# Kernel optimization log

Measured on AMD Instinct MI355X. Metric: run time of the kernel, lower is better.

The kernel has to match this reference:

```python
import jax, jax.numpy as jnp
import numpy as np

NEG_INF = -1e30  # stand-in for float('-inf'); avoids NaNs if a row is fully masked


def setup_inputs() -> dict:
    key = jax.random.key(0)
    k1, k2, k3, k4 = jax.random.split(key, 4)
    B, Q, K, D = 16, 2048, 2048, 64
    query = jax.random.normal(k1, (B, Q, D), dtype=jnp.float32)
    key_t = jax.random.normal(k2, (B, K, D), dtype=jnp.float32)
    value = jax.random.normal(k3, (B, K, D), dtype=jnp.float32)
    mask = jax.random.randint(k4, (B, Q, K), 0, 2).astype(jnp.bool_)
    return {"query": query, "key": key_t, "value": value, "mask": mask}


def reference(query, key, value, mask):
    d = query.shape[-1]
    # [B,Q,K] score matrix (naive attention, as in the original module)
    score = jnp.einsum('bqd,bkd->bqk', query, key) / jnp.sqrt(jnp.asarray(d, query.dtype))
    score = jnp.where(mask, NEG_INF, score)  # masked_fill(mask, -inf)
    attn = jax.nn.softmax(score, axis=-1)
    # dropout p=0.0 -> identity
    return jnp.einsum('bqk,bkd->bqd', attn, value)
```

## Files before the change

kernel.cpp:

```cpp
#include <hip/hip_runtime.h>


#define Bn   16
#define Qn   2048
#define Kseq 2048
#define Dn   64
#define QBLK 128
#define NEGF (-1e30f)

typedef __attribute__((ext_vector_type(8)))  short short8;
typedef __attribute__((ext_vector_type(16))) float f32x16;

static __device__ __forceinline__ short f2bf(float x) {
  union { float f; unsigned u; } un; un.f = x;
  unsigned r = un.u + 0x7FFFu + ((un.u >> 16) & 1u);
  return (short)(r >> 16);
}
static __device__ __forceinline__ unsigned pkbf(float lo, float hi) {
  unsigned r;
  asm("v_cvt_pk_bf16_f32 %0, %1, %2" : "=v"(r) : "v"(lo), "v"(hi));
  return r;
}
#if __has_builtin(__builtin_amdgcn_exp2f)
#define EXP2 __builtin_amdgcn_exp2f
#else
#define EXP2 exp2f
#endif
#define MFMA32 __builtin_amdgcn_mfma_f32_32x32x16_bf16

#define PREFETCH(MNXT)                                                        \
  do {                                                                        \
    ka0 = *(const float4*)(kp);                                               \
    ka1 = *(const float4*)(kp + 4);                                           \
    kb0 = *(const float4*)(kp + 2048);                                        \
    kb1 = *(const float4*)(kp + 2052);                                        \
    _Pragma("unroll")                                                         \
    for (int j = 0; j < 16; ++j) vreg[j] = vp[j * 64];                        \
    _Pragma("unroll")                                                         \
    for (int g = 0; g < 8; ++g) MNXT[g] = mp[2 * g];                          \
    kp += 4096; vp += 4096; mp += 16;                                         \
  } while (0)

#define WRITELDS()                                                            \
  do {                                                                        \
    short8 t;                                                                 \
    t[0]=f2bf(ka0.x); t[1]=f2bf(ka0.y); t[2]=f2bf(ka0.z); t[3]=f2bf(ka0.w);   \
    t[4]=f2bf(ka1.x); t[5]=f2bf(ka1.y); t[6]=f2bf(ka1.z); t[7]=f2bf(ka1.w);   \
    *(short8*)kwa = t;                                                        \
    t[0]=f2bf(kb0.x); t[1]=f2bf(kb0.y); t[2]=f2bf(kb0.z); t[3]=f2bf(kb0.w);   \
    t[4]=f2bf(kb1.x); t[5]=f2bf(kb1.y); t[6]=f2bf(kb1.z); t[7]=f2bf(kb1.w);   \
    *(short8*)kwb = t;                                                        \
    short8 v0, v1;                                                            \
    _Pragma("unroll")                                                         \
    for (int j = 0; j < 8; ++j) { v0[j]=f2bf(vreg[j]); v1[j]=f2bf(vreg[8+j]); } \
    *(short8*)vwa = v0; *(short8*)vwb = v1;                                   \
  } while (0)

#define COMPUTE(MCUR)                                                         \
  do {                                                                        \
    f32x16 st0, st1;                                                          \
    _Pragma("unroll")                                                         \
    for (int i = 0; i < 16; ++i) { st0[i] = 0.f; st1[i] = 0.f; }              \
    _Pragma("unroll")                                                         \
    for (int s = 0; s < 4; ++s) {                                             \
      short8 kf = *(const short8*)(krd + ((32*s + hh) ^ swz));                \
      st0 = MFMA32(kf, qf[s], st0, 0, 0, 0);                                  \
      short8 kg = *(const short8*)(krd + 4096 + ((32*s + hh) ^ swz));         \
      st1 = MFMA32(kg, qf[s], st1, 0, 0, 0);                                  \
    }                                                                         \
    float p0[16], p1[16];                                                     \
    _Pragma("unroll")                                                         \
    for (int g = 0; g < 4; ++g) {                                             \
      int4 m0 = MCUR[g]; int4 m1 = MCUR[4 + g];                               \
      p0[4*g+0] = m0.x ? NEGF : st0[4*g+0];                                   \
      p0[4*g+1] = m0.y ? NEGF : st0[4*g+1];                                   \
      p0[4*g+2] = m0.z ? NEGF : st0[4*g+2];                                   \
      p0[4*g+3] = m0.w ? NEGF : st0[4*g+3];                                   \
      p1[4*g+0] = m1.x ? NEGF : st1[4*g+0];                                   \
      p1[4*g+1] = m1.y ? NEGF : st1[4*g+1];                                   \
      p1[4*g+2] = m1.z ? NEGF : st1[4*g+2];                                   \
      p1[4*g+3] = m1.w ? NEGF : st1[4*g+3];                                   \
    }                                                                         \
    float mx8[8];                                                             \
    _Pragma("unroll")                                                         \
    for (int i = 0; i < 8; ++i)                                               \
      mx8[i] = fmaxf(fmaxf(p0[i], p0[i+8]), fmaxf(p1[i], p1[i+8]));           \
    float mx = fmaxf(fmaxf(fmaxf(mx8[0],mx8[1]), fmaxf(mx8[2],mx8[3])),       \
                     fmaxf(fmaxf(mx8[4],mx8[5]), fmaxf(mx8[6],mx8[7])));      \
    mx = fmaxf(mx, __shfl_xor(mx, 32));                                       \
    if (!__all(mx <= mrun)) {                                                 \
      float mnew  = fmaxf(mrun, mx);                                          \
      float alpha = EXP2(mrun - mnew);                                        \
      lrun *= alpha;                                                          \
      _Pragma("unroll")                                                       \
      for (int i = 0; i < 16; ++i) { ot0[i] *= alpha; ot1[i] *= alpha; }      \
      mrun = mnew;                                                            \
    }                                                                         \
    _Pragma("unroll")                                                         \
    for (int i = 0; i < 16; ++i) {                                            \
      p0[i] = EXP2(p0[i] - mrun);                                             \
      p1[i] = EXP2(p1[i] - mrun);                                             \
    }                                                                         \
    float s8[8];                                                              \
    _Pragma("unroll")                                                         \
    for (int i = 0; i < 8; ++i) s8[i] = (p0[i]+p0[i+8]) + (p1[i]+p1[i+8]);    \
    float lsum = ((s8[0]+s8[1]) + (s8[2]+s8[3])) +                            \
                 ((s8[4]+s8[5]) + (s8[6]+s8[7]));                             \
    lsum += __shfl_xor(lsum, 32);                                             \
    lrun += lsum;                                                             \
    union U8 { unsigned u[4]; short8 s; } f0, f1, f2, f3;                     \
    {                                                                         \
      unsigned x0 = pkbf(p0[0],p0[1]),   x1 = pkbf(p0[2],p0[3]);              \
      unsigned y0 = pkbf(p0[4],p0[5]),   y1 = pkbf(p0[6],p0[7]);              \
      unsigned a0 = pkbf(p0[8],p0[9]),   a1 = pkbf(p0[10],p0[11]);            \
      unsigned b0 = pkbf(p0[12],p0[13]), b1 = pkbf(p0[14],p0[15]);            \
      unsigned sx0 = __shfl_xor(x0,32), sx1 = __shfl_xor(x1,32);              \
      unsigned sy0 = __shfl_xor(y0,32), sy1 = __shfl_xor(y1,32);              \
      unsigned sa0 = __shfl_xor(a0,32), sa1 = __shfl_xor(a1,32);              \
      unsigned sb0 = __shfl_xor(b0,32), sb1 = __shfl_xor(b1,32);              \
      f0.u[0] = h ? sy0 : x0;  f0.u[1] = h ? sy1 : x1;                        \
      f0.u[2] = h ? y0 : sx0;  f0.u[3] = h ? y1 : sx1;                        \
      f1.u[0] = h ? sb0 : a0;  f1.u[1] = h ? sb1 : a1;                        \
      f1.u[2] = h ? b0 : sa0;  f1.u[3] = h ? b1 : sa1;                        \
    }                                                                         \
    {                                                                         \
      unsigned x0 = pkbf(p1[0],p1[1]),   x1 = pkbf(p1[2],p1[3]);              \
      unsigned y0 = pkbf(p1[4],p1[5]),   y1 = pkbf(p1[6],p1[7]);              \
      unsigned a0 = pkbf(p1[8],p1[9]),   a1 = pkbf(p1[10],p1[11]);            \
      unsigned b0 = pkbf(p1[12],p1[13]), b1 = pkbf(p1[14],p1[15]);            \
      unsigned sx0 = __shfl_xor(x0,32), sx1 = __shfl_xor(x1,32);              \
      unsigned sy0 = __shfl_xor(y0,32), sy1 = __shfl_xor(y1,32);              \
      unsigned sa0 = __shfl_xor(a0,32), sa1 = __shfl_xor(a1,32);              \
      unsigned sb0 = __shfl_xor(b0,32), sb1 = __shfl_xor(b1,32);              \
      f2.u[0] = h ? sy0 : x0;  f2.u[1] = h ? sy1 : x1;                        \
      f2.u[2] = h ? y0 : sx0;  f2.u[3] = h ? y1 : sx1;                        \
      f3.u[0] = h ? sb0 : a0;  f3.u[1] = h ? sb1 : a1;                        \
      f3.u[2] = h ? b0 : sa0;  f3.u[3] = h ? b1 : sa1;                        \
    }                                                                         \
    _Pragma("unroll")                                                         \
    for (int s = 0; s < 4; ++s) {                                             \
      short8 pf = (s==0) ? f0.s : (s==1) ? f1.s : (s==2) ? f2.s : f3.s;       \
      short8 va = *(const short8*)(vrd + ((32*s + hh) ^ swz));                \
      ot0 = MFMA32(va, pf, ot0, 0, 0, 0);                                     \
      short8 vb = *(const short8*)(vrd + 4096 + ((32*s + hh) ^ swz));         \
      ot1 = MFMA32(vb, pf, ot1, 0, 0, 0);                                     \
    }                                                                         \
  } while (0)

__launch_bounds__(256, 1)
__global__ void attn_fused(const float* __restrict__ Qg,
                           const float* __restrict__ Kg,
                           const float* __restrict__ Vg,
                           const int*   __restrict__ Mg,
                           float* __restrict__ Og) {
  __shared__ short8 lds8[1024];
  char* ldsb = (char*)lds8;

  const int tid  = threadIdx.x;
  const int lane = tid & 63;
  const int w    = tid >> 6;
  const int l31  = lane & 31;
  const int h    = lane >> 5;
  const int hh   = h << 4;
  const int swz  = (l31 & 7) << 4;
  const int b    = blockIdx.y;
  const int qb   = blockIdx.x * QBLK;
  const int q    = qb + w * 32 + l31;

  const float qscale = 0.18033688011112042f;
  const float* qp = Qg + ((size_t)(b * Qn + q)) * Dn + 8 * h;
  short8 qf[4];
#pragma unroll
  for (int s = 0; s < 4; ++s) {
    float4 a = *(const float4*)(qp + 16 * s);
    float4 c = *(const float4*)(qp + 16 * s + 4);
    short8 f;
    f[0]=f2bf(a.x*qscale); f[1]=f2bf(a.y*qscale); f[2]=f2bf(a.z*qscale); f[3]=f2bf(a.w*qscale);
    f[4]=f2bf(c.x*qscale); f[5]=f2bf(c.y*qscale); f[6]=f2bf(c.z*qscale); f[7]=f2bf(c.w*qscale);
    qf[s] = f;
  }

  const int krow = tid >> 3, kc8 = tid & 7;
  const float* kp = Kg + ((size_t)b * Kseq + krow) * Dn + kc8 * 8;
  const int vd = tid >> 2, vkc = (tid & 3) << 4;
  const float* vp = Vg + ((size_t)b * Kseq + vkc) * Dn + vd;
  char* kwa = ldsb + krow * 128 + ((kc8 * 16) ^ ((krow & 7) << 4));
  char* kwb = kwa + 32 * 128;
  char* vwa = ldsb + 8192 + vd * 128 + (((vkc * 2)     ) ^ ((vd & 7) << 4));
  char* vwb = ldsb + 8192 + vd * 128 + (((vkc * 2) + 16) ^ ((vd & 7) << 4));
  const char* krd = ldsb + l31 * 128;
  const char* vrd = ldsb + 8192 + l31 * 128;

  const int4* mp = (const int4*)(Mg + ((size_t)(b * Qn + q)) * Kseq) + h;

  f32x16 ot0, ot1;
#pragma unroll
  for (int i = 0; i < 16; ++i) { ot0[i] = 0.f; ot1[i] = 0.f; }
  float mrun = NEGF, lrun = 0.f;

  float4 ka0, ka1, kb0, kb1;
  float  vreg[16];
  int4   ma[8], mb[8];

  PREFETCH(ma);
  WRITELDS();
  __syncthreads();

#pragma unroll 1
  for (int kt = 0; kt < 32; kt += 2) {
    PREFETCH(mb);
    COMPUTE(ma);
    __syncthreads();
    WRITELDS();
    __syncthreads();
    if (kt + 1 < 31) { PREFETCH(ma); }
    COMPUTE(mb);
    __syncthreads();
    if (kt + 1 < 31) { WRITELDS(); }
    __syncthreads();
  }

  float inv = 1.0f / lrun;
  float* op = Og + ((size_t)(b * Qn + q)) * Dn;
#pragma unroll
  for (int g = 0; g < 4; ++g) {
    float4 o;
    o.x = ot0[4*g+0] * inv; o.y = ot0[4*g+1] * inv;
    o.z = ot0[4*g+2] * inv; o.w = ot0[4*g+3] * inv;
    *(float4*)(op + 8*g + 4*h) = o;
    o.x = ot1[4*g+0] * inv; o.y = ot1[4*g+1] * inv;
    o.z = ot1[4*g+2] * inv; o.w = ot1[4*g+3] * inv;
    *(float4*)(op + 32 + 8*g + 4*h) = o;
  }
}

extern "C" void kernel_launch(void* const* d_in, const int* in_sizes, int n_in,
                              void* d_out, int out_size, void* d_ws, size_t ws_size,
                              hipStream_t stream) {
  const float* Q = (const float*)d_in[0];
  const float* K = (const float*)d_in[1];
  const float* V = (const float*)d_in[2];
  const int*   M = (const int*)d_in[3];
  float* O = (float*)d_out;
  dim3 grid(Qn / QBLK, Bn);
  attn_fused<<<grid, dim3(256), 0, stream>>>(Q, K, V, M, O);
}
```

Baseline: 413.2 us.

## Split key range across two wave groups per block with LDS merge of softmax states

Blocks grow from 256 to 512 threads. Two groups of four waves each process alternating 64-key tiles for the same 128 queries, and their online-softmax states (max, sum, output) are merged through LDS at the end. The mask is loaded once per step and compressed into a 32-bit bitmask, replacing the double-buffered int4 mask registers. K/V staging is reorganized so that the single-buffered 32KB LDS holds two K and two V tiles per iteration, which halves the loop count. This raises waves in flight to hide the memory latency of the large mask stream, at the cost of an extra merge phase, more syncs, and register pressure under launch bounds of 512 threads with 2 blocks.

```diff
diff --git a/kernel.cpp b/kernel.cpp
--- a/kernel.cpp
+++ b/kernel.cpp
@@ -8,7 +8,9 @@
 #define QBLK 128
 #define NEGF (-1e30f)
 
+typedef __attribute__((ext_vector_type(4)))  short short4v;
 typedef __attribute__((ext_vector_type(8)))  short short8;
+typedef __attribute__((ext_vector_type(4)))  unsigned uint4v;
 typedef __attribute__((ext_vector_type(16))) float f32x16;
 
 static __device__ __forceinline__ short f2bf(float x) {
@@ -28,63 +30,70 @@
 #endif
 #define MFMA32 __builtin_amdgcn_mfma_f32_32x32x16_bf16
 
-#define PREFETCH(MNXT)                                                        \
-  do {                                                                        \
-    ka0 = *(const float4*)(kp);                                               \
-    ka1 = *(const float4*)(kp + 4);                                           \
-    kb0 = *(const float4*)(kp + 2048);                                        \
-    kb1 = *(const float4*)(kp + 2052);                                        \
-    _Pragma("unroll")                                                         \
-    for (int j = 0; j < 16; ++j) vreg[j] = vp[j * 64];                        \
-    _Pragma("unroll")                                                         \
-    for (int g = 0; g < 8; ++g) MNXT[g] = mp[2 * g];                          \
-    kp += 4096; vp += 4096; mp += 16;                                         \
+#define PREF_KV()                                                             \
+  do {                                                                        \
+    kst[0] = kp4[co0]; kst[1] = kp4[co1];                                     \
+    kst[2] = kp4[co2]; kst[3] = kp4[co3];                                     \
+    _Pragma("unroll")                                                         \
+    for (int j2 = 0; j2 < 8; ++j2) vst[j2] = *(const float2*)(vp + j2 * 64);  \
+    kp4 += 2048; vp += 8192;                                                  \
+  } while (0)
+
+#define PREF_M()                                                              \
+  do {                                                                        \
+    _Pragma("unroll")                                                         \
+    for (int g = 0; g < 8; ++g) ma[g] = mp[2 * g];                            \
+    mp += 32;                                                                 \
   } while (0)
 
 #define WRITELDS()                                                            \
   do {                                                                        \
-    short8 t;                                                                 \
-    t[0]=f2bf(ka0.x); t[1]=f2bf(ka0.y); t[2]=f2bf(ka0.z); t[3]=f2bf(ka0.w);   \
-    t[4]=f2bf(ka1.x); t[5]=f2bf(ka1.y); t[6]=f2bf(ka1.z); t[7]=f2bf(ka1.w);   \
-    *(short8*)kwa = t;                                                        \
-    t[0]=f2bf(kb0.x); t[1]=f2bf(kb0.y); t[2]=f2bf(kb0.z); t[3]=f2bf(kb0.w);   \
-    t[4]=f2bf(kb1.x); t[5]=f2bf(kb1.y); t[6]=f2bf(kb1.z); t[7]=f2bf(kb1.w);   \
-    *(short8*)kwb = t;                                                        \
+    _Pragma("unroll")                                                         \
+    for (int i = 0; i < 4; ++i) {                                             \
+      float4 a = kst[i]; short4v t;                                           \
+      t[0] = f2bf(a.x); t[1] = f2bf(a.y); t[2] = f2bf(a.z); t[3] = f2bf(a.w); \
+      *(short4v*)kdst[i] = t;                                                 \
+    }                                                                         \
     short8 v0, v1;                                                            \
     _Pragma("unroll")                                                         \
-    for (int j = 0; j < 8; ++j) { v0[j]=f2bf(vreg[j]); v1[j]=f2bf(vreg[8+j]); } \
-    *(short8*)vwa = v0; *(short8*)vwb = v1;                                   \
-  } while (0)
-
-#define COMPUTE(MCUR)                                                         \
+    for (int j2 = 0; j2 < 8; ++j2) { v0[j2] = f2bf(vst[j2].x); v1[j2] = f2bf(vst[j2].y); } \
+    *(short8*)vdst0 = v0; *(short8*)vdst1 = v1;                               \
+  } while (0)
+
+static __device__ __forceinline__ unsigned compress_mask(const int4* ma) {
+  unsigned bits = 0;
+#pragma unroll
+  for (int g = 0; g < 8; ++g) {
+    int4 m = ma[g];
+    const int sh = ((g & 4) << 2) + ((g & 3) << 2);
+    unsigned bsel = (m.x != 0 ? 1u : 0u) | (m.y != 0 ? 2u : 0u) |
+                    (m.z != 0 ? 4u : 0u) | (m.w != 0 ? 8u : 0u);
+    bits |= bsel << sh;
+  }
+  return bits;
+}
+
+#define COMPUTE()                                                             \
   do {                                                                        \
     f32x16 st0, st1;                                                          \
     _Pragma("unroll")                                                         \
     for (int i = 0; i < 16; ++i) { st0[i] = 0.f; st1[i] = 0.f; }              \
     _Pragma("unroll")                                                         \
     for (int s = 0; s < 4; ++s) {                                             \
-      short8 kf = *(const short8*)(krd + ((32*s + hh) ^ swz));                \
+      short8 kf = *(const short8*)(krd + ((32 * s + hh) ^ swz));              \
       st0 = MFMA32(kf, qf[s], st0, 0, 0, 0);                                  \
-      short8 kg = *(const short8*)(krd + 4096 + ((32*s + hh) ^ swz));         \
+      short8 kg = *(const short8*)(krd + 4096 + ((32 * s + hh) ^ swz));       \
       st1 = MFMA32(kg, qf[s], st1, 0, 0, 0);                                  \
     }                                                                         \
-    float p0[16], p1[16];                                                     \
-    _Pragma("unroll")                                                         \
-    for (int g = 0; g < 4; ++g) {                                             \
-      int4 m0 = MCUR[g]; int4 m1 = MCUR[4 + g];                               \
-      p0[4*g+0] = m0.x ? NEGF : st0[4*g+0];                                   \
-      p0[4*g+1] = m0.y ? NEGF : st0[4*g+1];                                   \
-      p0[4*g+2] = m0.z ? NEGF : st0[4*g+2];                                   \
-      p0[4*g+3] = m0.w ? NEGF : st0[4*g+3];                                   \
-      p1[4*g+0] = m1.x ? NEGF : st1[4*g+0];                                   \
-      p1[4*g+1] = m1.y ? NEGF : st1[4*g+1];                                   \
-      p1[4*g+2] = m1.z ? NEGF : st1[4*g+2];                                   \
-      p1[4*g+3] = m1.w ? NEGF : st1[4*g+3];                                   \
+    _Pragma("unroll")                                                         \
+    for (int i = 0; i < 16; ++i) {                                            \
+      st0[i] = (bits & (1u << i))       ? NEGF : st0[i];                      \
+      st1[i] = (bits & (0x10000u << i)) ? NEGF : st1[i];                      \
     }                                                                         \
     float mx8[8];                                                             \
     _Pragma("unroll")                                                         \
     for (int i = 0; i < 8; ++i)                                               \
-      mx8[i] = fmaxf(fmaxf(p0[i], p0[i+8]), fmaxf(p1[i], p1[i+8]));           \
+      mx8[i] = fmaxf(fmaxf(st0[i], st0[i+8]), fmaxf(st1[i], st1[i+8]));       \
     float mx = fmaxf(fmaxf(fmaxf(mx8[0],mx8[1]), fmaxf(mx8[2],mx8[3])),       \
                      fmaxf(fmaxf(mx8[4],mx8[5]), fmaxf(mx8[6],mx8[7])));      \
     mx = fmaxf(mx, __shfl_xor(mx, 32));                                       \
@@ -98,74 +107,75 @@
     }                                                                         \
     _Pragma("unroll")                                                         \
     for (int i = 0; i < 16; ++i) {                                            \
-      p0[i] = EXP2(p0[i] - mrun);                                             \
-      p1[i] = EXP2(p1[i] - mrun);                                             \
+      st0[i] = EXP2(st0[i] - mrun);                                           \
+      st1[i] = EXP2(st1[i] - mrun);                                           \
     }                                                                         \
     float s8[8];                                                              \
     _Pragma("unroll")                                                         \
-    for (int i = 0; i < 8; ++i) s8[i] = (p0[i]+p0[i+8]) + (p1[i]+p1[i+8]);    \
+    for (int i = 0; i < 8; ++i) s8[i] = (st0[i]+st0[i+8]) + (st1[i]+st1[i+8]);\
     float lsum = ((s8[0]+s8[1]) + (s8[2]+s8[3])) +                            \
                  ((s8[4]+s8[5]) + (s8[6]+s8[7]));                             \
     lsum += __shfl_xor(lsum, 32);                                             \
     lrun += lsum;                                                             \
-    union U8 { unsigned u[4]; short8 s; } f0, f1, f2, f3;                     \
+    short8 f0, f1, f2, f3;                                                    \
     {                                                                         \
-      unsigned x0 = pkbf(p0[0],p0[1]),   x1 = pkbf(p0[2],p0[3]);              \
-      unsigned y0 = pkbf(p0[4],p0[5]),   y1 = pkbf(p0[6],p0[7]);              \
-      unsigned a0 = pkbf(p0[8],p0[9]),   a1 = pkbf(p0[10],p0[11]);            \
-      unsigned b0 = pkbf(p0[12],p0[13]), b1 = pkbf(p0[14],p0[15]);            \
+      unsigned x0 = pkbf(st0[0],st0[1]),   x1 = pkbf(st0[2],st0[3]);          \
+      unsigned y0 = pkbf(st0[4],st0[5]),   y1 = pkbf(st0[6],st0[7]);          \
+      unsigned a0 = pkbf(st0[8],st0[9]),   a1 = pkbf(st0[10],st0[11]);        \
+      unsigned b0 = pkbf(st0[12],st0[13]), b1 = pkbf(st0[14],st0[15]);        \
       unsigned sx0 = __shfl_xor(x0,32), sx1 = __shfl_xor(x1,32);              \
       unsigned sy0 = __shfl_xor(y0,32), sy1 = __shfl_xor(y1,32);              \
       unsigned sa0 = __shfl_xor(a0,32), sa1 = __shfl_xor(a1,32);              \
       unsigned sb0 = __shfl_xor(b0,32), sb1 = __shfl_xor(b1,32);              \
-      f0.u[0] = h ? sy0 : x0;  f0.u[1] = h ? sy1 : x1;                        \
-      f0.u[2] = h ? y0 : sx0;  f0.u[3] = h ? y1 : sx1;                        \
-      f1.u[0] = h ? sb0 : a0;  f1.u[1] = h ? sb1 : a1;                        \
-      f1.u[2] = h ? b0 : sa0;  f1.u[3] = h ? b1 : sa1;                        \
+      uint4v u0 = { h ? sy0 : x0, h ? sy1 : x1, h ? y0 : sx0, h ? y1 : sx1 }; \
+      uint4v u1 = { h ? sb0 : a0, h ? sb1 : a1, h ? b0 : sa0, h ? b1 : sa1 }; \
+      f0 = __builtin_bit_cast(short8, u0);                                    \
+      f1 = __builtin_bit_cast(short8, u1);                                    \
     }                                                                         \
     {                                                                         \
-      unsigned x0 = pkbf(p1[0],p1[1]),   x1 = pkbf(p1[2],p1[3]);              \
-      unsigned y0 = pkbf(p1[4],p1[5]),   y1 = pkbf(p1[6],p1[7]);              \
-      unsigned a0 = pkbf(p1[8],p1[9]),   a1 = pkbf(p1[10],p1[11]);            \
-      unsigned b0 = pkbf(p1[12],p1[13]), b1 = pkbf(p1[14],p1[15]);            \
+      unsigned x0 = pkbf(st1[0],st1[1]),   x1 = pkbf(st1[2],st1[3]);          \
+      unsigned y0 = pkbf(st1[4],st1[5]),   y1 = pkbf(st1[6],st1[7]);          \
+      unsigned a0 = pkbf(st1[8],st1[9]),   a1 = pkbf(st1[10],st1[11]);        \
+      unsigned b0 = pkbf(st1[12],st1[13]), b1 = pkbf(st1[14],st1[15]);        \
       unsigned sx0 = __shfl_xor(x0,32), sx1 = __shfl_xor(x1,32);              \
       unsigned sy0 = __shfl_xor(y0,32), sy1 = __shfl_xor(y1,32);              \
       unsigned sa0 = __shfl_xor(a0,32), sa1 = __shfl_xor(a1,32);              \
       unsigned sb0 = __shfl_xor(b0,32), sb1 = __shfl_xor(b1,32);              \
-      f2.u[0] = h ? sy0 : x0;  f2.u[1] = h ? sy1 : x1;                        \
-      f2.u[2] = h ? y0 : sx0;  f2.u[3] = h ? y1 : sx1;                        \
-      f3.u[0] = h ? sb0 : a0;  f3.u[1] = h ? sb1 : a1;                        \
-      f3.u[2] = h ? b0 : sa0;  f3.u[3] = h ? b1 : sa1;                        \
+      uint4v u2 = { h ? sy0 : x0, h ? sy1 : x1, h ? y0 : sx0, h ? y1 : sx1 }; \
+      uint4v u3 = { h ? sb0 : a0, h ? sb1 : a1, h ? b0 : sa0, h ? b1 : sa1 }; \
+      f2 = __builtin_bit_cast(short8, u2);                                    \
+      f3 = __builtin_bit_cast(short8, u3);                                    \
     }                                                                         \
     _Pragma("unroll")                                                         \
     for (int s = 0; s < 4; ++s) {                                             \
-      short8 pf = (s==0) ? f0.s : (s==1) ? f1.s : (s==2) ? f2.s : f3.s;       \
-      short8 va = *(const short8*)(vrd + ((32*s + hh) ^ swz));                \
+      short8 pf = (s==0) ? f0 : (s==1) ? f1 : (s==2) ? f2 : f3;               \
+      short8 va = *(const short8*)(vrd + ((32 * s + hh) ^ swz));              \
       ot0 = MFMA32(va, pf, ot0, 0, 0, 0);                                     \
-      short8 vb = *(const short8*)(vrd + 4096 + ((32*s + hh) ^ swz));         \
+      short8 vb = *(const short8*)(vrd + 4096 + ((32 * s + hh) ^ swz));       \
       ot1 = MFMA32(vb, pf, ot1, 0, 0, 0);                                     \
     }                                                                         \
   } while (0)
 
-__launch_bounds__(256, 1)
+__launch_bounds__(512, 2)
 __global__ void attn_fused(const float* __restrict__ Qg,
                            const float* __restrict__ Kg,
                            const float* __restrict__ Vg,
                            const int*   __restrict__ Mg,
                            float* __restrict__ Og) {
-  __shared__ short8 lds8[1024];
-  char* ldsb = (char*)lds8;
+  __shared__ char ldsb[32768];
 
   const int tid  = threadIdx.x;
   const int lane = tid & 63;
   const int w    = tid >> 6;
+  const int wq   = w & 3;
+  const int grp  = w >> 2;
   const int l31  = lane & 31;
   const int h    = lane >> 5;
   const int hh   = h << 4;
   const int swz  = (l31 & 7) << 4;
   const int b    = blockIdx.y;
   const int qb   = blockIdx.x * QBLK;
-  const int q    = qb + w * 32 + l31;
+  const int q    = qb + wq * 32 + l31;
 
   const float qscale = 0.18033688011112042f;
   const float* qp = Qg + ((size_t)(b * Qn + q)) * Dn + 8 * h;
@@ -180,57 +190,99 @@
     qf[s] = f;
   }
 
-  const int krow = tid >> 3, kc8 = tid & 7;
-  const float* kp = Kg + ((size_t)b * Kseq + krow) * Dn + kc8 * 8;
-  const int vd = tid >> 2, vkc = (tid & 3) << 4;
-  const float* vp = Vg + ((size_t)b * Kseq + vkc) * Dn + vd;
-  char* kwa = ldsb + krow * 128 + ((kc8 * 16) ^ ((krow & 7) << 4));
-  char* kwb = kwa + 32 * 128;
-  char* vwa = ldsb + 8192 + vd * 128 + (((vkc * 2)     ) ^ ((vd & 7) << 4));
-  char* vwb = ldsb + 8192 + vd * 128 + (((vkc * 2) + 16) ^ ((vd & 7) << 4));
-  const char* krd = ldsb + l31 * 128;
-  const char* vrd = ldsb + 8192 + l31 * 128;
-
-  const int4* mp = (const int4*)(Mg + ((size_t)(b * Qn + q)) * Kseq) + h;
+  const float4* kp4 = (const float4*)(Kg + (size_t)b * Kseq * Dn);
+  const int co0 = tid, co1 = tid + 512, co2 = tid + 1024, co3 = tid + 1536;
+  char* kdst[4];
+#pragma unroll
+  for (int i = 0; i < 4; ++i) {
+    int c = tid + 512 * i;
+    int row = c >> 4, col16 = c & 15;
+    int tile = row >> 6, r = row & 63;
+    kdst[i] = ldsb + tile * 8192 + r * 128 +
+              (((col16 >> 1) << 4) ^ ((r & 7) << 4)) + ((col16 & 1) << 3);
+  }
+
+  const int uu = tid & 255, tileV = tid >> 8;
+  const int d0 = (uu & 31) * 2, kv8 = (uu >> 5) * 8;
+  const float* vp = Vg + ((size_t)b * Kseq + tileV * 64 + kv8) * Dn + d0;
+  char* vdst0 = ldsb + 16384 + tileV * 8192 + d0 * 128 + ((kv8 * 2) ^ ((d0 & 7) << 4));
+  char* vdst1 = ldsb + 16384 + tileV * 8192 + (d0 + 1) * 128 + ((kv8 * 2) ^ (((d0 + 1) & 7) << 4));
+
+  const int4* mp = (const int4*)(Mg + ((size_t)(b * Qn + q)) * Kseq) + 16 * grp + h;
+
+  const char* krd = ldsb + grp * 8192 + l31 * 128;
+  const char* vrd = ldsb + 16384 + grp * 8192 + l31 * 128;
 
   f32x16 ot0, ot1;
 #pragma unroll
   for (int i = 0; i < 16; ++i) { ot0[i] = 0.f; ot1[i] = 0.f; }
   float mrun = NEGF, lrun = 0.f;
 
-  float4 ka0, ka1, kb0, kb1;
-  float  vreg[16];
-  int4   ma[8], mb[8];
-
-  PREFETCH(ma);
+  float4 kst[4];
+  float2 vst[8];
+  int4   ma[8];
+  unsigned bits;
+
+  PREF_KV();
+  PREF_M();
   WRITELDS();
+  bits = compress_mask(ma);
   __syncthreads();
 
 #pragma unroll 1
-  for (int kt = 0; kt < 32; kt += 2) {
-    PREFETCH(mb);
-    COMPUTE(ma);
-    __syncthreads();
-    WRITELDS();
-    __syncthreads();
-    if (kt + 1 < 31) { PREFETCH(ma); }
-    COMPUTE(mb);
-    __syncthreads();
-    if (kt + 1 < 31) { WRITELDS(); }
-    __syncthreads();
-  }
-
-  float inv = 1.0f / lrun;
-  float* op = Og + ((size_t)(b * Qn + q)) * Dn;
-#pragma unroll
-  for (int g = 0; g < 4; ++g) {
-    float4 o;
-    o.x = ot0[4*g+0] * inv; o.y = ot0[4*g+1] * inv;
-    o.z = ot0[4*g+2] * inv; o.w = ot0[4*g+3] * inv;
-    *(float4*)(op + 8*g + 4*h) = o;
-    o.x = ot1[4*g+0] * inv; o.y = ot1[4*g+1] * inv;
-    o.z = ot1[4*g+2] * inv; o.w = ot1[4*g+3] * inv;
-    *(float4*)(op + 32 + 8*g + 4*h) = o;
+  for (int j = 0; j < 16; ++j) {
+    if (j < 15) { PREF_KV(); PREF_M(); }
+    COMPUTE();
+    if (j < 15) {
+      bits = compress_mask(ma);
+      __syncthreads();
+      WRITELDS();
+      __syncthreads();
+    }
+  }
+
+  __syncthreads();
+
+  float* lm = (float*)ldsb;
+  float* ll = lm + 256;
+  float* lo = ll + 256;
+  const int s4 = wq * 64 + lane;
+  if (grp == 1) {
+    lm[s4] = mrun; ll[s4] = lrun;
+#pragma unroll
+    for (int i = 0; i < 16; ++i) lo[s4 * 20 + i] = ot0[i];
+  }
+  __syncthreads();
+  float aA = 1.f, aB = 0.f;
+  if (grp == 0) {
+    float mB = lm[s4], lB = ll[s4];
+    float ms = fmaxf(mrun, mB);
+    aA = EXP2(mrun - ms); aB = EXP2(mB - ms);
+    lrun = lrun * aA + lB * aB;
+#pragma unroll
+    for (int i = 0; i < 16; ++i) ot0[i] = ot0[i] * aA + lo[s4 * 20 + i] * aB;
+  }
+  __syncthreads();
+  if (grp == 1) {
+#pragma unroll
+    for (int i = 0; i < 16; ++i) lo[s4 * 20 + i] = ot1[i];
+  }
+  __syncthreads();
+  if (grp == 0) {
+#pragma unroll
+    for (int i = 0; i < 16; ++i) ot1[i] = ot1[i] * aA + lo[s4 * 20 + i] * aB;
+    float inv = 1.0f / lrun;
+    float* op = Og + ((size_t)(b * Qn + q)) * Dn;
+#pragma unroll
+    for (int g = 0; g < 4; ++g) {
+      float4 o;
+      o.x = ot0[4*g+0] * inv; o.y = ot0[4*g+1] * inv;
+      o.z = ot0[4*g+2] * inv; o.w = ot0[4*g+3] * inv;
+      *(float4*)(op + 8*g + 4*h) = o;
+      o.x = ot1[4*g+0] * inv; o.y = ot1[4*g+1] * inv;
+      o.z = ot1[4*g+2] * inv; o.w = ot1[4*g+3] * inv;
+      *(float4*)(op + 32 + 8*g + 4*h) = o;
+    }
   }
 }
 
@@ -243,5 +295,5 @@
   const int*   M = (const int*)d_in[3];
   float* O = (float*)d_out;
   dim3 grid(Qn / QBLK, Bn);
-  attn_fused<<<grid, dim3(256), 0, stream>>>(Q, K, V, M, O);
-}
+  attn_fused<<<grid, dim3(512), 0, stream>>>(Q, K, V, M, O);
+}
```

After: 409.2 us. No clear change (-1.0%).
